# Performance work log

Hardware: AMD Instinct MI355X
Metric: run time of the kernel (lower is better)

## Reference

```python
import jax, jax.numpy as jnp
import numpy as np

N_NODES = 50000
N_EDGES = 800000
D_FEAT = 128
UNITS = 128


def setup_inputs() -> dict:
    key = jax.random.key(0)
    k1, k2, k3, k4 = jax.random.split(key, 4)
    x = jax.random.normal(k1, (N_NODES, D_FEAT), dtype=jnp.float32)
    source = jax.random.randint(k2, (N_EDGES,), 0, N_NODES, dtype=jnp.int32)
    target = jax.random.randint(k3, (N_EDGES,), 0, N_NODES, dtype=jnp.int32)
    W = jax.random.normal(k4, (D_FEAT, UNITS), dtype=jnp.float32) * (1.0 / np.sqrt(D_FEAT))
    b = jnp.zeros((UNITS,), dtype=jnp.float32)
    return {"x": x, "source": source, "target": target, "W": W, "b": b}


def _degree(idx, n_nodes):
    # in/out degree = segment-sum of unit edge weights; clamp to >= 1 (no self loops)
    deg = jnp.zeros((n_nodes,), dtype=jnp.float32).at[idx].add(1.0)
    return jnp.maximum(deg, 1.0)


def reference(x, source, target, W, b):
    n = x.shape[0]
    # degree_normalization == "in_out": sender scale from out-degree, receiver from in-degree
    sender_scale = jax.lax.rsqrt(_degree(source, n))[:, None]      # [N, 1]
    receiver_scale = jax.lax.rsqrt(_degree(target, n))[:, None]    # [N, 1]
    normalized = sender_scale * x                                  # [N, D]
    source_bcast = normalized[source]                              # [E, D] gather
    pooled = jax.ops.segment_sum(source_bcast, target, num_segments=n)  # [N, D] scatter-add
    pooled = receiver_scale * pooled
    # Dense(units, activation='relu', use_bias=True)
    return jax.nn.relu(pooled @ W + b)
```

## Files before the change

### kernel.cpp

```cpp
#include <hip/hip_runtime.h>
#include <hip/hip_bf16.h>

#define N_FEAT 128
#define EPT 8
#define CHUNK 2048
#define BSHIFT 8
#define MAXRANGE 256
#define CAP 8192
#define LSTR 66

typedef short bf16x8 __attribute__((ext_vector_type(8)));
typedef float f32x4  __attribute__((ext_vector_type(4)));

__device__ __forceinline__ unsigned short f2bf_rtne(float f) {
    unsigned u = __float_as_uint(f);
    u += 0x7fffu + ((u >> 16) & 1u);
    return (unsigned short)(u >> 16);
}
__device__ __forceinline__ float bf2f(unsigned short h) {
    return __uint_as_float((unsigned)h << 16);
}

__global__ __launch_bounds__(256) void scatter_kernel(const int* __restrict__ source,
                                                      const int* __restrict__ target,
                                                      int* __restrict__ curT,
                                                      int* __restrict__ curS,
                                                      unsigned int* __restrict__ pairsT,
                                                      unsigned char* __restrict__ srcB,
                                                      int E, int NB) {
    __shared__ unsigned int   lds_pairs[CHUNK];
    __shared__ unsigned short lds_sp[CHUNK];
    __shared__ int ct[MAXRANGE], cs[MAXRANGE];
    __shared__ int st[MAXRANGE], ss[MAXRANGE];
    __shared__ int gt[MAXRANGE], gs[MAXRANGE];
    int tid = threadIdx.x, b = blockIdx.x;
    int base = b * CHUNK;
    int cnt = E - base; if (cnt > CHUNK) cnt = CHUNK;

    int rs[EPT], rt[EPT];
    ct[tid] = 0; cs[tid] = 0;
    __syncthreads();
    #pragma unroll
    for (int j = 0; j < EPT; ++j) {
        int e = base + j * 256 + tid;
        if (e < E) {
            int s = source[e], t = target[e];
            rs[j] = s; rt[j] = t;
            atomicAdd(&ct[t >> BSHIFT], 1);
            atomicAdd(&cs[s >> BSHIFT], 1);
        }
    }
    __syncthreads();
    int vt = ct[tid], vs = cs[tid];
    st[tid] = vt; ss[tid] = vs;
    __syncthreads();
    #pragma unroll
    for (int off = 1; off < 256; off <<= 1) {
        int t1 = (tid >= off) ? st[tid - off] : 0;
        int t2 = (tid >= off) ? ss[tid - off] : 0;
        __syncthreads();
        st[tid] += t1; ss[tid] += t2;
        __syncthreads();
    }
    int et = st[tid] - vt, es = ss[tid] - vs;
    int gT = 0, gS = 0;
    if (tid < NB) {
        if (vt) gT = atomicAdd(&curT[tid], vt);
        if (vs) gS = atomicAdd(&curS[tid], vs);
    }
    __syncthreads();
    st[tid] = et; ss[tid] = es;
    ct[tid] = et; cs[tid] = es;
    gt[tid] = gT; gs[tid] = gS;
    __syncthreads();
    #pragma unroll
    for (int j = 0; j < EPT; ++j) {
        int e = base + j * 256 + tid;
        if (e < E) {
            int s = rs[j], t = rt[j];
            int k = t >> BSHIFT;
            int p = atomicAdd(&ct[k], 1);
            lds_pairs[p] = (unsigned)s | ((unsigned)t << 16);
            int k2 = s >> BSHIFT;
            int p2 = atomicAdd(&cs[k2], 1);
            lds_sp[p2] = (unsigned short)s;
        }
    }
    __syncthreads();
    for (int i = tid; i < cnt; i += 256) {
        unsigned w = lds_pairs[i];
        int k = w >> 24;
        pairsT[(size_t)k * CAP + gt[k] + (i - st[k])] = w;
        unsigned short sp = lds_sp[i];
        int k2 = sp >> 8;
        srcB[(size_t)k2 * CAP + gs[k2] + (i - ss[k2])] = (unsigned char)sp;
    }
}

__global__ __launch_bounds__(256) void prep_kernel(const unsigned char* __restrict__ srcB,
                                                   const unsigned int* __restrict__ pairsT,
                                                   const int* __restrict__ curT,
                                                   const int* __restrict__ curS,
                                                   const float* __restrict__ x,
                                                   const float* __restrict__ W,
                                                   unsigned short* __restrict__ xb,
                                                   int2* __restrict__ offs,
                                                   int* __restrict__ elist,
                                                   float* __restrict__ ri,
                                                   unsigned short* __restrict__ Whi,
                                                   unsigned short* __restrict__ Wlo,
                                                   int N, int NB) {
    __shared__ int hist[MAXRANGE];
    __shared__ int sb[MAXRANGE];
    __shared__ int excl[MAXRANGE];
    __shared__ int cur[MAXRANGE];
    __shared__ float so_l[MAXRANGE];
    int tid = threadIdx.x, b = blockIdx.x;

    if (b < NB) {
        hist[tid] = 0;
        __syncthreads();
        int cnt = curS[b];
        size_t base = (size_t)b * CAP;
        for (int i = tid; i < cnt; i += 256)
            atomicAdd(&hist[srcB[base + i]], 1);
        __syncthreads();
        {
            int d = hist[tid]; if (d < 1) d = 1;
            so_l[tid] = rsqrtf((float)d);
        }
        __syncthreads();
        int row0 = b << BSHIFT;
        int nrows = N - row0; if (nrows > 256) nrows = 256;
        if (nrows <= 0) return;
        int nf4 = nrows * (N_FEAT / 4);
        const float4* xr = (const float4*)(x + (size_t)row0 * N_FEAT);
        ushort4* xo = (ushort4*)(xb + (size_t)row0 * N_FEAT);
        for (int i = tid; i < nf4; i += 256) {
            float s = so_l[i >> 5];
            float4 v = xr[i];
            xo[i] = make_ushort4(f2bf_rtne(s * v.x), f2bf_rtne(s * v.y),
                                 f2bf_rtne(s * v.z), f2bf_rtne(s * v.w));
        }
    } else if (b < 2 * NB) {
        int bb = b - NB;
        hist[tid] = 0; cur[tid] = 0;
        __syncthreads();
        int cnt = curT[bb];
        int gbase = bb * CAP;
        for (int i = tid; i < cnt; i += 256)
            atomicAdd(&hist[(pairsT[(size_t)gbase + i] >> 16) & 255], 1);
        __syncthreads();
        int deg = hist[tid];
        sb[tid] = deg;
        __syncthreads();
        #pragma unroll
        for (int off = 1; off < 256; off <<= 1) {
            int t = (tid >= off) ? sb[tid - off] : 0;
            __syncthreads();
            sb[tid] += t;
            __syncthreads();
        }
        excl[tid] = sb[tid] - deg;
        __syncthreads();
        int node = (bb << BSHIFT) + tid;
        if (node < N) {
            int st0 = gbase + excl[tid];
            offs[node] = make_int2(st0, st0 + deg);
            int d = deg; if (d < 1) d = 1;
            ri[node] = rsqrtf((float)d);
        }
        for (int i = tid; i < cnt; i += 256) {
            unsigned w = pairsT[(size_t)gbase + i];
            int tl = (w >> 16) & 255;
            int pos = atomicAdd(&cur[tl], 1);
            elist[gbase + excl[tl] + pos] = (int)(w & 0xFFFFu);
        }
    } else {
        int idx = (b - 2 * NB) * 256 + tid;
        int lane = idx & 63;
        int ks = (idx >> 6) & 3;
        int ct2 = idx >> 8;
        int n  = ct2 * 16 + (lane & 15);
        int k0 = ks * 32 + (lane >> 4) * 8;
        unsigned short h[8], l[8];
        #pragma unroll
        for (int j = 0; j < 8; ++j) {
            float w = W[(k0 + j) * N_FEAT + n];
            unsigned short hh = f2bf_rtne(w);
            h[j] = hh;
            l[j] = f2bf_rtne(w - bf2f(hh));
        }
        size_t off = (size_t)idx * 8;
        *(ushort4*)(Whi + off)     = make_ushort4(h[0], h[1], h[2], h[3]);
        *(ushort4*)(Whi + off + 4) = make_ushort4(h[4], h[5], h[6], h[7]);
        *(ushort4*)(Wlo + off)     = make_ushort4(l[0], l[1], l[2], l[3]);
        *(ushort4*)(Wlo + off + 4) = make_ushort4(l[4], l[5], l[6], l[7]);
    }
}

__global__ __launch_bounds__(256) void agg_gemm_kernel(const unsigned short* __restrict__ xb,
                                                       const int* __restrict__ elist,
                                                       const int2* __restrict__ offs,
                                                       const float* __restrict__ ri,
                                                       const unsigned short* __restrict__ Whi,
                                                       const unsigned short* __restrict__ Wlo,
                                                       const float* __restrict__ bias,
                                                       float* __restrict__ out,
                                                       int N) {
    __shared__ unsigned int hi_l[16 * LSTR];
    __shared__ unsigned int lo_l[16 * LSTR];
    int wave = threadIdx.x >> 6;
    int lane = threadIdx.x & 63;
    int quad = lane >> 4;
    int rowbase = blockIdx.x * 16;
    int col = lane * 2;

    #pragma unroll
    for (int i = 0; i < 4; ++i) {
        int r = wave * 4 + i;
        int node = rowbase + r;
        float vx = 0.f, vy = 0.f;
        if (node < N) {
            int2 oe = offs[node];
            int start = oe.x, end = oe.y;
            float2 a0 = make_float2(0.f, 0.f), a1 = a0, a2 = a0, a3 = a0;
            int j = start;
            for (; j + 8 <= end; j += 8) {
                int e0 = __builtin_amdgcn_readfirstlane(elist[j]);
                int e1 = __builtin_amdgcn_readfirstlane(elist[j + 1]);
                int e2 = __builtin_amdgcn_readfirstlane(elist[j + 2]);
                int e3 = __builtin_amdgcn_readfirstlane(elist[j + 3]);
                int e4 = __builtin_amdgcn_readfirstlane(elist[j + 4]);
                int e5 = __builtin_amdgcn_readfirstlane(elist[j + 5]);
                int e6 = __builtin_amdgcn_readfirstlane(elist[j + 6]);
                int e7 = __builtin_amdgcn_readfirstlane(elist[j + 7]);
                unsigned u0 = *(const unsigned*)(xb + (size_t)e0 * N_FEAT + col);
                unsigned u1 = *(const unsigned*)(xb + (size_t)e1 * N_FEAT + col);
                unsigned u2 = *(const unsigned*)(xb + (size_t)e2 * N_FEAT + col);
                unsigned u3 = *(const unsigned*)(xb + (size_t)e3 * N_FEAT + col);
                unsigned u4 = *(const unsigned*)(xb + (size_t)e4 * N_FEAT + col);
                unsigned u5 = *(const unsigned*)(xb + (size_t)e5 * N_FEAT + col);
                unsigned u6 = *(const unsigned*)(xb + (size_t)e6 * N_FEAT + col);
                unsigned u7 = *(const unsigned*)(xb + (size_t)e7 * N_FEAT + col);
                a0.x += __uint_as_float(u0 << 16); a0.y += __uint_as_float(u0 & 0xffff0000u);
                a1.x += __uint_as_float(u1 << 16); a1.y += __uint_as_float(u1 & 0xffff0000u);
                a2.x += __uint_as_float(u2 << 16); a2.y += __uint_as_float(u2 & 0xffff0000u);
                a3.x += __uint_as_float(u3 << 16); a3.y += __uint_as_float(u3 & 0xffff0000u);
                a0.x += __uint_as_float(u4 << 16); a0.y += __uint_as_float(u4 & 0xffff0000u);
                a1.x += __uint_as_float(u5 << 16); a1.y += __uint_as_float(u5 & 0xffff0000u);
                a2.x += __uint_as_float(u6 << 16); a2.y += __uint_as_float(u6 & 0xffff0000u);
                a3.x += __uint_as_float(u7 << 16); a3.y += __uint_as_float(u7 & 0xffff0000u);
            }
            for (; j < end; ++j) {
                int e = __builtin_amdgcn_readfirstlane(elist[j]);
                unsigned u = *(const unsigned*)(xb + (size_t)e * N_FEAT + col);
                a0.x += __uint_as_float(u << 16); a0.y += __uint_as_float(u & 0xffff0000u);
            }
            float rr = ri[node];
            vx = ((a0.x + a1.x) + (a2.x + a3.x)) * rr;
            vy = ((a0.y + a1.y) + (a2.y + a3.y)) * rr;
        }
        unsigned short hx = f2bf_rtne(vx), hy = f2bf_rtne(vy);
        unsigned short lx = f2bf_rtne(vx - bf2f(hx)), ly = f2bf_rtne(vy - bf2f(hy));
        hi_l[r * LSTR + lane] = (unsigned)hx | ((unsigned)hy << 16);
        lo_l[r * LSTR + lane] = (unsigned)lx | ((unsigned)ly << 16);
    }
    __syncthreads();

    bf16x8 Ahi[4], Alo[4];
    int m = lane & 15;
    #pragma unroll
    for (int ks = 0; ks < 4; ++ks) {
        int a = m * LSTR + ks * 16 + quad * 4;
        Ahi[ks] = *(const bf16x8*)(hi_l + a);
        Alo[ks] = *(const bf16x8*)(lo_l + a);
    }
    const bf16x8* BH = (const bf16x8*)Whi;
    const bf16x8* BL = (const bf16x8*)Wlo;

    #pragma unroll
    for (int c = 0; c < 2; ++c) {
        int ct = wave * 2 + c;
        f32x4 acc = {0.f, 0.f, 0.f, 0.f};
        #pragma unroll
        for (int ks = 0; ks < 4; ++ks) {
            bf16x8 bh = BH[(ct * 4 + ks) * 64 + lane];
            bf16x8 bl = BL[(ct * 4 + ks) * 64 + lane];
            acc = __builtin_amdgcn_mfma_f32_16x16x32_bf16(Ahi[ks], bh, acc, 0, 0, 0);
            acc = __builtin_amdgcn_mfma_f32_16x16x32_bf16(Alo[ks], bh, acc, 0, 0, 0);
            acc = __builtin_amdgcn_mfma_f32_16x16x32_bf16(Ahi[ks], bl, acc, 0, 0, 0);
        }
        int colc = ct * 16 + m;
        float bv = bias[colc];
        #pragma unroll
        for (int reg = 0; reg < 4; ++reg) {
            int r = rowbase + quad * 4 + reg;
            if (r < N)
                out[(size_t)r * N_FEAT + colc] = fmaxf(acc[reg] + bv, 0.f);
        }
    }
}

extern "C" void kernel_launch(void* const* d_in, const int* in_sizes, int n_in,
                              void* d_out, int out_size, void* d_ws, size_t ws_size,
                              hipStream_t stream) {
    const float* x      = (const float*)d_in[0];
    const int*   source = (const int*)d_in[1];
    const int*   target = (const int*)d_in[2];
    const float* W      = (const float*)d_in[3];
    const float* bias   = (const float*)d_in[4];
    float*       out    = (float*)d_out;

    const int N = in_sizes[0] / N_FEAT;
    const int E = in_sizes[1];

    const int NB   = (N + MAXRANGE - 1) >> BSHIFT;
    const int NBLK = (E + CHUNK - 1) / CHUNK;

    uintptr_t p = (uintptr_t)d_ws;
    auto carve = [&](size_t bytes) {
        p = (p + 255) & ~(uintptr_t)255;
        uintptr_t r = p;
        p += bytes;
        return (void*)r;
    };
    int*            curs    = (int*)carve((size_t)2 * NB * sizeof(int));
    int*            curT    = curs;
    int*            curS    = curs + NB;
    unsigned int*   pairsT  = (unsigned int*)carve((size_t)NB * CAP * sizeof(unsigned int));
    int*            elist   = (int*)carve((size_t)NB * CAP * sizeof(int));
    unsigned char*  srcB    = (unsigned char*)carve((size_t)NB * CAP);
    float*          ri      = (float*)carve((size_t)N * sizeof(float));
    int2*           offs    = (int2*)carve((size_t)N * sizeof(int2));
    unsigned short* xb      = (unsigned short*)carve((size_t)N * N_FEAT * sizeof(unsigned short));
    unsigned short* Whi     = (unsigned short*)carve((size_t)N_FEAT * N_FEAT * sizeof(unsigned short));
    unsigned short* Wlo     = (unsigned short*)carve((size_t)N_FEAT * N_FEAT * sizeof(unsigned short));
    (void)ws_size; (void)n_in; (void)out_size;

    (void)hipMemsetAsync(curs, 0, (size_t)2 * NB * sizeof(int), stream);

    scatter_kernel<<<NBLK, 256, 0, stream>>>(source, target, curT, curS, pairsT, srcB, E, NB);
    prep_kernel<<<2 * NB + 8, 256, 0, stream>>>(srcB, pairsT, curT, curS, x, W,
                                                xb, offs, elist, ri, Whi, Wlo, N, NB);
    agg_gemm_kernel<<<(N + 15) / 16, 256, 0, stream>>>(xb, elist, offs, ri,
                                                       Whi, Wlo, bias, out, N);
}
```

Measured before the change: 168.2 us.

## Interleave four-row gathers with padded CSR and per-wave histogram scans

Rebuilds the edge lists so each node's segment is padded to a multiple of four with a sentinel index pointing at a zeroed extra row of xb. This lets the aggregation kernel load indices as int4 and interleave the gathers of all four rows a wave owns, putting many independent loads in flight. The scatter and prep kernels switch to per-wave LDS histograms with shuffle-based wave scans instead of barrier-heavy block scans, halve the chunk size, and read source bytes as 32-bit words. Padding adds some wasted gathers of the zero row, and the interleaved loop runs to the longest of the four rows.

```diff
diff --git a/kernel.cpp b/kernel.cpp
--- a/kernel.cpp
+++ b/kernel.cpp
@@ -2,8 +2,8 @@
 #include <hip/hip_bf16.h>
 
 #define N_FEAT 128
-#define EPT 8
-#define CHUNK 2048
+#define EPT 4
+#define CHUNK 1024
 #define BSHIFT 8
 #define MAXRANGE 256
 #define CAP 8192
@@ -19,6 +19,14 @@
 }
 __device__ __forceinline__ float bf2f(unsigned short h) {
     return __uint_as_float((unsigned)h << 16);
+}
+__device__ __forceinline__ int wave_incl_scan(int v, int lane) {
+    #pragma unroll
+    for (int d = 1; d < 64; d <<= 1) {
+        int t = __shfl_up(v, d);
+        if (lane >= d) v += t;
+    }
+    return v;
 }
 
 __global__ __launch_bounds__(256) void scatter_kernel(const int* __restrict__ source,
@@ -28,69 +36,77 @@
                                                       unsigned int* __restrict__ pairsT,
                                                       unsigned char* __restrict__ srcB,
                                                       int E, int NB) {
+    __shared__ int ht[4][MAXRANGE];
+    __shared__ int hs[4][MAXRANGE];
     __shared__ unsigned int   lds_pairs[CHUNK];
     __shared__ unsigned short lds_sp[CHUNK];
-    __shared__ int ct[MAXRANGE], cs[MAXRANGE];
     __shared__ int st[MAXRANGE], ss[MAXRANGE];
     __shared__ int gt[MAXRANGE], gs[MAXRANGE];
-    int tid = threadIdx.x, b = blockIdx.x;
+    __shared__ int cwT[4][MAXRANGE], cwS[4][MAXRANGE];
+    __shared__ int wsumT[4], wsumS[4];
+    int tid = threadIdx.x, lane = tid & 63, w = tid >> 6, b = blockIdx.x;
     int base = b * CHUNK;
     int cnt = E - base; if (cnt > CHUNK) cnt = CHUNK;
 
+    #pragma unroll
+    for (int i = 0; i < 4; ++i) { ht[i][tid] = 0; hs[i][tid] = 0; }
+    __syncthreads();
     int rs[EPT], rt[EPT];
-    ct[tid] = 0; cs[tid] = 0;
-    __syncthreads();
     #pragma unroll
     for (int j = 0; j < EPT; ++j) {
         int e = base + j * 256 + tid;
         if (e < E) {
             int s = source[e], t = target[e];
             rs[j] = s; rt[j] = t;
-            atomicAdd(&ct[t >> BSHIFT], 1);
-            atomicAdd(&cs[s >> BSHIFT], 1);
-        }
-    }
-    __syncthreads();
-    int vt = ct[tid], vs = cs[tid];
-    st[tid] = vt; ss[tid] = vs;
-    __syncthreads();
-    #pragma unroll
-    for (int off = 1; off < 256; off <<= 1) {
-        int t1 = (tid >= off) ? st[tid - off] : 0;
-        int t2 = (tid >= off) ? ss[tid - off] : 0;
-        __syncthreads();
-        st[tid] += t1; ss[tid] += t2;
-        __syncthreads();
-    }
-    int et = st[tid] - vt, es = ss[tid] - vs;
+            atomicAdd(&ht[w][t >> BSHIFT], 1);
+            atomicAdd(&hs[w][s >> BSHIFT], 1);
+        }
+    }
+    __syncthreads();
+    int k = tid;
+    int h0 = ht[0][k], h1 = ht[1][k], h2 = ht[2][k], h3 = ht[3][k];
+    int hT = h0 + h1 + h2 + h3;
+    int q0 = hs[0][k], q1 = hs[1][k], q2 = hs[2][k], q3 = hs[3][k];
+    int hS = q0 + q1 + q2 + q3;
+    int iT = wave_incl_scan(hT, lane);
+    int iS = wave_incl_scan(hS, lane);
+    if (lane == 63) { wsumT[w] = iT; wsumS[w] = iS; }
+    __syncthreads();
+    int bT = 0, bS = 0;
+    #pragma unroll
+    for (int i = 0; i < 4; ++i) if (i < w) { bT += wsumT[i]; bS += wsumS[i]; }
+    int exclT = bT + iT - hT;
+    int exclS = bS + iS - hS;
     int gT = 0, gS = 0;
-    if (tid < NB) {
-        if (vt) gT = atomicAdd(&curT[tid], vt);
-        if (vs) gS = atomicAdd(&curS[tid], vs);
-    }
-    __syncthreads();
-    st[tid] = et; ss[tid] = es;
-    ct[tid] = et; cs[tid] = es;
-    gt[tid] = gT; gs[tid] = gS;
+    if (k < NB) {
+        if (hT) gT = atomicAdd(&curT[k], hT);
+        if (hS) gS = atomicAdd(&curS[k], hS);
+    }
+    st[k] = exclT; ss[k] = exclS;
+    gt[k] = gT;    gs[k] = gS;
+    cwT[0][k] = exclT;                cwS[0][k] = exclS;
+    cwT[1][k] = exclT + h0;           cwS[1][k] = exclS + q0;
+    cwT[2][k] = exclT + h0 + h1;      cwS[2][k] = exclS + q0 + q1;
+    cwT[3][k] = exclT + h0 + h1 + h2; cwS[3][k] = exclS + q0 + q1 + q2;
     __syncthreads();
     #pragma unroll
     for (int j = 0; j < EPT; ++j) {
         int e = base + j * 256 + tid;
         if (e < E) {
             int s = rs[j], t = rt[j];
-            int k = t >> BSHIFT;
-            int p = atomicAdd(&ct[k], 1);
+            int kk = t >> BSHIFT;
+            int p = atomicAdd(&cwT[w][kk], 1);
             lds_pairs[p] = (unsigned)s | ((unsigned)t << 16);
             int k2 = s >> BSHIFT;
-            int p2 = atomicAdd(&cs[k2], 1);
+            int p2 = atomicAdd(&cwS[w][k2], 1);
             lds_sp[p2] = (unsigned short)s;
         }
     }
     __syncthreads();
     for (int i = tid; i < cnt; i += 256) {
-        unsigned w = lds_pairs[i];
-        int k = w >> 24;
-        pairsT[(size_t)k * CAP + gt[k] + (i - st[k])] = w;
+        unsigned ww = lds_pairs[i];
+        int kk = ww >> 24;
+        pairsT[(size_t)kk * CAP + gt[kk] + (i - st[kk])] = ww;
         unsigned short sp = lds_sp[i];
         int k2 = sp >> 8;
         srcB[(size_t)k2 * CAP + gs[k2] + (i - ss[k2])] = (unsigned char)sp;
@@ -110,23 +126,32 @@
                                                    unsigned short* __restrict__ Whi,
                                                    unsigned short* __restrict__ Wlo,
                                                    int N, int NB) {
-    __shared__ int hist[MAXRANGE];
-    __shared__ int sb[MAXRANGE];
-    __shared__ int excl[MAXRANGE];
-    __shared__ int cur[MAXRANGE];
+    __shared__ int h4[4][MAXRANGE];
+    __shared__ int cw4[4][MAXRANGE];
     __shared__ float so_l[MAXRANGE];
-    int tid = threadIdx.x, b = blockIdx.x;
+    __shared__ int wsum[4];
+    int tid = threadIdx.x, lane = tid & 63, w = tid >> 6, b = blockIdx.x;
 
     if (b < NB) {
-        hist[tid] = 0;
+        #pragma unroll
+        for (int i = 0; i < 4; ++i) h4[i][tid] = 0;
         __syncthreads();
         int cnt = curS[b];
-        size_t base = (size_t)b * CAP;
-        for (int i = tid; i < cnt; i += 256)
-            atomicAdd(&hist[srcB[base + i]], 1);
+        const unsigned* p32 = (const unsigned*)(srcB + (size_t)b * CAP);
+        int nw = cnt >> 2;
+        for (int i = tid; i < nw; i += 256) {
+            unsigned v = p32[i];
+            atomicAdd(&h4[w][v & 255], 1);
+            atomicAdd(&h4[w][(v >> 8) & 255], 1);
+            atomicAdd(&h4[w][(v >> 16) & 255], 1);
+            atomicAdd(&h4[w][v >> 24], 1);
+        }
+        if (tid < (cnt & 3))
+            atomicAdd(&h4[w][srcB[(size_t)b * CAP + nw * 4 + tid]], 1);
         __syncthreads();
         {
-            int d = hist[tid]; if (d < 1) d = 1;
+            int d = h4[0][tid] + h4[1][tid] + h4[2][tid] + h4[3][tid];
+            if (d < 1) d = 1;
             so_l[tid] = rsqrtf((float)d);
         }
         __syncthreads();
@@ -144,60 +169,70 @@
         }
     } else if (b < 2 * NB) {
         int bb = b - NB;
-        hist[tid] = 0; cur[tid] = 0;
+        #pragma unroll
+        for (int i = 0; i < 4; ++i) h4[i][tid] = 0;
         __syncthreads();
         int cnt = curT[bb];
         int gbase = bb * CAP;
         for (int i = tid; i < cnt; i += 256)
-            atomicAdd(&hist[(pairsT[(size_t)gbase + i] >> 16) & 255], 1);
-        __syncthreads();
-        int deg = hist[tid];
-        sb[tid] = deg;
-        __syncthreads();
-        #pragma unroll
-        for (int off = 1; off < 256; off <<= 1) {
-            int t = (tid >= off) ? sb[tid - off] : 0;
-            __syncthreads();
-            sb[tid] += t;
-            __syncthreads();
-        }
-        excl[tid] = sb[tid] - deg;
-        __syncthreads();
+            atomicAdd(&h4[w][(pairsT[(size_t)gbase + i] >> 16) & 255], 1);
+        __syncthreads();
+        int d0 = h4[0][tid], d1 = h4[1][tid], d2 = h4[2][tid], d3 = h4[3][tid];
+        int deg = d0 + d1 + d2 + d3;
+        int pdeg = (deg + 3) & ~3;
+        int incl = wave_incl_scan(pdeg, lane);
+        if (lane == 63) wsum[w] = incl;
+        __syncthreads();
+        int basew = 0;
+        #pragma unroll
+        for (int i = 0; i < 4; ++i) if (i < w) basew += wsum[i];
+        int ex = basew + incl - pdeg;
+        cw4[0][tid] = ex;
+        cw4[1][tid] = ex + d0;
+        cw4[2][tid] = ex + d0 + d1;
+        cw4[3][tid] = ex + d0 + d1 + d2;
         int node = (bb << BSHIFT) + tid;
         if (node < N) {
-            int st0 = gbase + excl[tid];
-            offs[node] = make_int2(st0, st0 + deg);
-            int d = deg; if (d < 1) d = 1;
-            ri[node] = rsqrtf((float)d);
-        }
+            offs[node] = make_int2(gbase + ex, gbase + ex + pdeg);
+            int dd = deg; if (dd < 1) dd = 1;
+            ri[node] = rsqrtf((float)dd);
+        }
+        for (int p = deg; p < pdeg; ++p)
+            elist[gbase + ex + p] = N;
+        __syncthreads();
         for (int i = tid; i < cnt; i += 256) {
-            unsigned w = pairsT[(size_t)gbase + i];
-            int tl = (w >> 16) & 255;
-            int pos = atomicAdd(&cur[tl], 1);
-            elist[gbase + excl[tl] + pos] = (int)(w & 0xFFFFu);
-        }
-    } else {
+            unsigned ww = pairsT[(size_t)gbase + i];
+            int tl = (ww >> 16) & 255;
+            int pos = atomicAdd(&cw4[w][tl], 1);
+            elist[gbase + pos] = (int)(ww & 0xFFFFu);
+        }
+    } else if (b < 2 * NB + 8) {
         int idx = (b - 2 * NB) * 256 + tid;
-        int lane = idx & 63;
+        int ln = idx & 63;
         int ks = (idx >> 6) & 3;
         int ct2 = idx >> 8;
-        int n  = ct2 * 16 + (lane & 15);
-        int k0 = ks * 32 + (lane >> 4) * 8;
+        int n  = ct2 * 16 + (ln & 15);
+        int k0 = ks * 32 + (ln >> 4) * 8;
         unsigned short h[8], l[8];
         #pragma unroll
         for (int j = 0; j < 8; ++j) {
-            float w = W[(k0 + j) * N_FEAT + n];
-            unsigned short hh = f2bf_rtne(w);
+            float wv = W[(k0 + j) * N_FEAT + n];
+            unsigned short hh = f2bf_rtne(wv);
             h[j] = hh;
-            l[j] = f2bf_rtne(w - bf2f(hh));
+            l[j] = f2bf_rtne(wv - bf2f(hh));
         }
         size_t off = (size_t)idx * 8;
         *(ushort4*)(Whi + off)     = make_ushort4(h[0], h[1], h[2], h[3]);
         *(ushort4*)(Whi + off + 4) = make_ushort4(h[4], h[5], h[6], h[7]);
         *(ushort4*)(Wlo + off)     = make_ushort4(l[0], l[1], l[2], l[3]);
         *(ushort4*)(Wlo + off + 4) = make_ushort4(l[4], l[5], l[6], l[7]);
-    }
-}
+    } else {
+        if (tid < 64) ((unsigned*)(xb + (size_t)N * N_FEAT))[tid] = 0;
+    }
+}
+
+#define ACC_ROW(u, a) { a.x += __uint_as_float((u) << 16); \
+                        a.y += __uint_as_float((u) & 0xffff0000u); }
 
 __global__ __launch_bounds__(256) void agg_gemm_kernel(const unsigned short* __restrict__ xb,
                                                        const int* __restrict__ elist,
@@ -216,55 +251,89 @@
     int rowbase = blockIdx.x * 16;
     int col = lane * 2;
 
-    #pragma unroll
-    for (int i = 0; i < 4; ++i) {
-        int r = wave * 4 + i;
-        int node = rowbase + r;
-        float vx = 0.f, vy = 0.f;
-        if (node < N) {
-            int2 oe = offs[node];
-            int start = oe.x, end = oe.y;
-            float2 a0 = make_float2(0.f, 0.f), a1 = a0, a2 = a0, a3 = a0;
-            int j = start;
-            for (; j + 8 <= end; j += 8) {
-                int e0 = __builtin_amdgcn_readfirstlane(elist[j]);
-                int e1 = __builtin_amdgcn_readfirstlane(elist[j + 1]);
-                int e2 = __builtin_amdgcn_readfirstlane(elist[j + 2]);
-                int e3 = __builtin_amdgcn_readfirstlane(elist[j + 3]);
-                int e4 = __builtin_amdgcn_readfirstlane(elist[j + 4]);
-                int e5 = __builtin_amdgcn_readfirstlane(elist[j + 5]);
-                int e6 = __builtin_amdgcn_readfirstlane(elist[j + 6]);
-                int e7 = __builtin_amdgcn_readfirstlane(elist[j + 7]);
-                unsigned u0 = *(const unsigned*)(xb + (size_t)e0 * N_FEAT + col);
-                unsigned u1 = *(const unsigned*)(xb + (size_t)e1 * N_FEAT + col);
-                unsigned u2 = *(const unsigned*)(xb + (size_t)e2 * N_FEAT + col);
-                unsigned u3 = *(const unsigned*)(xb + (size_t)e3 * N_FEAT + col);
-                unsigned u4 = *(const unsigned*)(xb + (size_t)e4 * N_FEAT + col);
-                unsigned u5 = *(const unsigned*)(xb + (size_t)e5 * N_FEAT + col);
-                unsigned u6 = *(const unsigned*)(xb + (size_t)e6 * N_FEAT + col);
-                unsigned u7 = *(const unsigned*)(xb + (size_t)e7 * N_FEAT + col);
-                a0.x += __uint_as_float(u0 << 16); a0.y += __uint_as_float(u0 & 0xffff0000u);
-                a1.x += __uint_as_float(u1 << 16); a1.y += __uint_as_float(u1 & 0xffff0000u);
-                a2.x += __uint_as_float(u2 << 16); a2.y += __uint_as_float(u2 & 0xffff0000u);
-                a3.x += __uint_as_float(u3 << 16); a3.y += __uint_as_float(u3 & 0xffff0000u);
-                a0.x += __uint_as_float(u4 << 16); a0.y += __uint_as_float(u4 & 0xffff0000u);
-                a1.x += __uint_as_float(u5 << 16); a1.y += __uint_as_float(u5 & 0xffff0000u);
-                a2.x += __uint_as_float(u6 << 16); a2.y += __uint_as_float(u6 & 0xffff0000u);
-                a3.x += __uint_as_float(u7 << 16); a3.y += __uint_as_float(u7 & 0xffff0000u);
-            }
-            for (; j < end; ++j) {
-                int e = __builtin_amdgcn_readfirstlane(elist[j]);
-                unsigned u = *(const unsigned*)(xb + (size_t)e * N_FEAT + col);
-                a0.x += __uint_as_float(u << 16); a0.y += __uint_as_float(u & 0xffff0000u);
-            }
-            float rr = ri[node];
-            vx = ((a0.x + a1.x) + (a2.x + a3.x)) * rr;
-            vy = ((a0.y + a1.y) + (a2.y + a3.y)) * rr;
-        }
+    int n0 = rowbase + wave * 4 + 0;
+    int n1 = rowbase + wave * 4 + 1;
+    int n2 = rowbase + wave * 4 + 2;
+    int n3 = rowbase + wave * 4 + 3;
+    int2 o0 = (n0 < N) ? offs[n0] : make_int2(0, 0);
+    int2 o1 = (n1 < N) ? offs[n1] : make_int2(0, 0);
+    int2 o2 = (n2 < N) ? offs[n2] : make_int2(0, 0);
+    int2 o3 = (n3 < N) ? offs[n3] : make_int2(0, 0);
+    int j0 = __builtin_amdgcn_readfirstlane(o0.x), e0v = __builtin_amdgcn_readfirstlane(o0.y);
+    int j1 = __builtin_amdgcn_readfirstlane(o1.x), e1v = __builtin_amdgcn_readfirstlane(o1.y);
+    int j2 = __builtin_amdgcn_readfirstlane(o2.x), e2v = __builtin_amdgcn_readfirstlane(o2.y);
+    int j3 = __builtin_amdgcn_readfirstlane(o3.x), e3v = __builtin_amdgcn_readfirstlane(o3.y);
+    float rr0 = (n0 < N) ? ri[n0] : 0.f;
+    float rr1 = (n1 < N) ? ri[n1] : 0.f;
+    float rr2 = (n2 < N) ? ri[n2] : 0.f;
+    float rr3 = (n3 < N) ? ri[n3] : 0.f;
+    float2 z = make_float2(0.f, 0.f);
+    float2 A0[4] = {z, z, z, z}, A1[4] = {z, z, z, z};
+    float2 A2[4] = {z, z, z, z}, A3[4] = {z, z, z, z};
+
+    while (j0 < e0v || j1 < e1v || j2 < e2v || j3 < e3v) {
+        int4 i0 = (j0 < e0v) ? *(const int4*)(elist + j0) : make_int4(N, N, N, N);
+        int4 i1 = (j1 < e1v) ? *(const int4*)(elist + j1) : make_int4(N, N, N, N);
+        int4 i2 = (j2 < e2v) ? *(const int4*)(elist + j2) : make_int4(N, N, N, N);
+        int4 i3 = (j3 < e3v) ? *(const int4*)(elist + j3) : make_int4(N, N, N, N);
+        unsigned u00 = *(const unsigned*)(xb + (size_t)i0.x * N_FEAT + col);
+        unsigned u01 = *(const unsigned*)(xb + (size_t)i0.y * N_FEAT + col);
+        unsigned u02 = *(const unsigned*)(xb + (size_t)i0.z * N_FEAT + col);
+        unsigned u03 = *(const unsigned*)(xb + (size_t)i0.w * N_FEAT + col);
+        unsigned u10 = *(const unsigned*)(xb + (size_t)i1.x * N_FEAT + col);
+        unsigned u11 = *(const unsigned*)(xb + (size_t)i1.y * N_FEAT + col);
+        unsigned u12 = *(const unsigned*)(xb + (size_t)i1.z * N_FEAT + col);
+        unsigned u13 = *(const unsigned*)(xb + (size_t)i1.w * N_FEAT + col);
+        unsigned u20 = *(const unsigned*)(xb + (size_t)i2.x * N_FEAT + col);
+        unsigned u21 = *(const unsigned*)(xb + (size_t)i2.y * N_FEAT + col);
+        unsigned u22 = *(const unsigned*)(xb + (size_t)i2.z * N_FEAT + col);
+        unsigned u23 = *(const unsigned*)(xb + (size_t)i2.w * N_FEAT + col);
+        unsigned u30 = *(const unsigned*)(xb + (size_t)i3.x * N_FEAT + col);
+        unsigned u31 = *(const unsigned*)(xb + (size_t)i3.y * N_FEAT + col);
+        unsigned u32r = *(const unsigned*)(xb + (size_t)i3.z * N_FEAT + col);
+        unsigned u33 = *(const unsigned*)(xb + (size_t)i3.w * N_FEAT + col);
+        ACC_ROW(u00, A0[0]) ACC_ROW(u01, A0[1]) ACC_ROW(u02, A0[2]) ACC_ROW(u03, A0[3])
+        ACC_ROW(u10, A1[0]) ACC_ROW(u11, A1[1]) ACC_ROW(u12, A1[2]) ACC_ROW(u13, A1[3])
+        ACC_ROW(u20, A2[0]) ACC_ROW(u21, A2[1]) ACC_ROW(u22, A2[2]) ACC_ROW(u23, A2[3])
+        ACC_ROW(u30, A3[0]) ACC_ROW(u31, A3[1]) ACC_ROW(u32r, A3[2]) ACC_ROW(u33, A3[3])
+        j0 += (j0 < e0v) ? 4 : 0;
+        j1 += (j1 < e1v) ? 4 : 0;
+        j2 += (j2 < e2v) ? 4 : 0;
+        j3 += (j3 < e3v) ? 4 : 0;
+    }
+
+    int rbase = wave * 4;
+    {
+        float vx = ((A0[0].x + A0[1].x) + (A0[2].x + A0[3].x)) * rr0;
+        float vy = ((A0[0].y + A0[1].y) + (A0[2].y + A0[3].y)) * rr0;
         unsigned short hx = f2bf_rtne(vx), hy = f2bf_rtne(vy);
         unsigned short lx = f2bf_rtne(vx - bf2f(hx)), ly = f2bf_rtne(vy - bf2f(hy));
-        hi_l[r * LSTR + lane] = (unsigned)hx | ((unsigned)hy << 16);
-        lo_l[r * LSTR + lane] = (unsigned)lx | ((unsigned)ly << 16);
+        hi_l[(rbase + 0) * LSTR + lane] = (unsigned)hx | ((unsigned)hy << 16);
+        lo_l[(rbase + 0) * LSTR + lane] = (unsigned)lx | ((unsigned)ly << 16);
+    }
+    {
+        float vx = ((A1[0].x + A1[1].x) + (A1[2].x + A1[3].x)) * rr1;
+        float vy = ((A1[0].y + A1[1].y) + (A1[2].y + A1[3].y)) * rr1;
+        unsigned short hx = f2bf_rtne(vx), hy = f2bf_rtne(vy);
+        unsigned short lx = f2bf_rtne(vx - bf2f(hx)), ly = f2bf_rtne(vy - bf2f(hy));
+        hi_l[(rbase + 1) * LSTR + lane] = (unsigned)hx | ((unsigned)hy << 16);
+        lo_l[(rbase + 1) * LSTR + lane] = (unsigned)lx | ((unsigned)ly << 16);
+    }
+    {
+        float vx = ((A2[0].x + A2[1].x) + (A2[2].x + A2[3].x)) * rr2;
+        float vy = ((A2[0].y + A2[1].y) + (A2[2].y + A2[3].y)) * rr2;
+        unsigned short hx = f2bf_rtne(vx), hy = f2bf_rtne(vy);
+        unsigned short lx = f2bf_rtne(vx - bf2f(hx)), ly = f2bf_rtne(vy - bf2f(hy));
+        hi_l[(rbase + 2) * LSTR + lane] = (unsigned)hx | ((unsigned)hy << 16);
+        lo_l[(rbase + 2) * LSTR + lane] = (unsigned)lx | ((unsigned)ly << 16);
+    }
+    {
+        float vx = ((A3[0].x + A3[1].x) + (A3[2].x + A3[3].x)) * rr3;
+        float vy = ((A3[0].y + A3[1].y) + (A3[2].y + A3[3].y)) * rr3;
+        unsigned short hx = f2bf_rtne(vx), hy = f2bf_rtne(vy);
+        unsigned short lx = f2bf_rtne(vx - bf2f(hx)), ly = f2bf_rtne(vy - bf2f(hy));
+        hi_l[(rbase + 3) * LSTR + lane] = (unsigned)hx | ((unsigned)hy << 16);
+        lo_l[(rbase + 3) * LSTR + lane] = (unsigned)lx | ((unsigned)ly << 16);
     }
     __syncthreads();
 
@@ -333,7 +402,7 @@
     unsigned char*  srcB    = (unsigned char*)carve((size_t)NB * CAP);
     float*          ri      = (float*)carve((size_t)N * sizeof(float));
     int2*           offs    = (int2*)carve((size_t)N * sizeof(int2));
-    unsigned short* xb      = (unsigned short*)carve((size_t)N * N_FEAT * sizeof(unsigned short));
+    unsigned short* xb      = (unsigned short*)carve((size_t)(N + 1) * N_FEAT * sizeof(unsigned short));
     unsigned short* Whi     = (unsigned short*)carve((size_t)N_FEAT * N_FEAT * sizeof(unsigned short));
     unsigned short* Wlo     = (unsigned short*)carve((size_t)N_FEAT * N_FEAT * sizeof(unsigned short));
     (void)ws_size; (void)n_in; (void)out_size;
@@ -341,7 +410,7 @@
     (void)hipMemsetAsync(curs, 0, (size_t)2 * NB * sizeof(int), stream);
 
     scatter_kernel<<<NBLK, 256, 0, stream>>>(source, target, curT, curS, pairsT, srcB, E, NB);
-    prep_kernel<<<2 * NB + 8, 256, 0, stream>>>(srcB, pairsT, curT, curS, x, W,
+    prep_kernel<<<2 * NB + 9, 256, 0, stream>>>(srcB, pairsT, curT, curS, x, W,
                                                 xb, offs, elist, ri, Whi, Wlo, N, NB);
     agg_gemm_kernel<<<(N + 15) / 16, 256, 0, stream>>>(xb, elist, offs, ri,
                                                        Whi, Wlo, bias, out, N);
```

Result: faster. 163.5 us (-2.8%).
